# Kernel optimization log

Hardware: AMD Instinct MI355X
Metric: run time of the kernel (lower is better)

The kernel has to match this reference:

```python
import jax, jax.numpy as jnp
import numpy as np

NEG_INF = -1.0e9  # matches torch masked_fill value


def setup_inputs() -> dict:
    key = jax.random.key(0)
    kq, kk, kv, km = jax.random.split(key, 4)
    B, S, D = 16, 2048, 256
    q = jax.random.normal(kq, (B, S, D), dtype=jnp.float32)
    k = jax.random.normal(kk, (B, D, S), dtype=jnp.float32)  # pre-transposed keys
    v = jax.random.normal(kv, (B, S, D), dtype=jnp.float32)
    mask = jax.random.randint(km, (B, 1, S), 0, 2, dtype=jnp.int32)
    return {"q": q, "k": k, "v": v, "mask": mask}


def reference(q, k, v, mask):
    # q: [B, n_q, d], k: [B, d, n_k], v: [B, n_k, n_dv]
    n_dk = k.shape[1]
    att = jnp.matmul(q, k)                      # [B, n_q, n_k]
    att = jnp.where(mask == 0, NEG_INF, att)    # masked_fill(mask==0, -1e9)
    # NOTE: faithful to source — scale applied AFTER softmax
    att = jax.nn.softmax(att, axis=-1) / jnp.asarray(n_dk, att.dtype) ** 0.5
    out = jnp.matmul(att, v)                    # [B, n_q, n_dv]
    return jnp.transpose(out, (0, 2, 1))        # [B, n_dv, n_q]
```

## Files before the change

### kernel.cpp

```cpp
#include <hip/hip_runtime.h>

typedef _Float16 half8 __attribute__((ext_vector_type(8)));
typedef float floatx16 __attribute__((ext_vector_type(16)));

#define B_  16
#define S_  2048
#define D_  256
#define P_RS 40
#define LOG2E 1.4426950408889634f

#define DPP_ROR(x, n) __int_as_float(__builtin_amdgcn_update_dpp( \
    0, __float_as_int(x), 0x120 + (n), 0xf, 0xf, false))

__device__ __forceinline__ float rmax32(float x) {
    x = fmaxf(x, DPP_ROR(x, 1));
    x = fmaxf(x, DPP_ROR(x, 2));
    x = fmaxf(x, DPP_ROR(x, 4));
    x = fmaxf(x, DPP_ROR(x, 8));
    x = fmaxf(x, __shfl_xor(x, 16, 64));
    return x;
}
__device__ __forceinline__ float rsum32(float x) {
    x += DPP_ROR(x, 1);
    x += DPP_ROR(x, 2);
    x += DPP_ROR(x, 4);
    x += DPP_ROR(x, 8);
    x += __shfl_xor(x, 16, 64);
    return x;
}

__device__ __forceinline__ void dma16(const _Float16* g, _Float16* l) {
    __builtin_amdgcn_global_load_lds(
        (const __attribute__((address_space(1))) void*)g,
        (__attribute__((address_space(3))) void*)l, 16, 0, 0);
}

__global__ __launch_bounds__(256)
void tr_swz(const float* __restrict__ in, _Float16* __restrict__ out,
            int Rin, int Cin, int swz)
{
    __shared__ _Float16 tl[64 * 72];
    const int t  = threadIdx.x;
    const int c0 = blockIdx.x * 64, r0 = blockIdx.y * 64;
    const float* ib = in  + (size_t)blockIdx.z * Rin * Cin;
    _Float16*    ob = out + (size_t)blockIdx.z * Rin * Cin;

    const int rr = t >> 4, cc = (t & 15) * 4;
    #pragma unroll
    for (int p = 0; p < 4; ++p) {
        const float4 x = *(const float4*)(ib + (size_t)(r0 + rr + 16*p) * Cin + c0 + cc);
        tl[(cc+0)*72 + rr + 16*p] = (_Float16)x.x;
        tl[(cc+1)*72 + rr + 16*p] = (_Float16)x.y;
        tl[(cc+2)*72 + rr + 16*p] = (_Float16)x.z;
        tl[(cc+3)*72 + rr + 16*p] = (_Float16)x.w;
    }
    __syncthreads();
    #pragma unroll
    for (int u = 0; u < 2; ++u) {
        const int idx  = t + 256*u;
        const int jloc = idx >> 3, lc = idx & 7;
        const half8 h = *(const half8*)(tl + jloc*72 + 8*lc);
        const int jg  = c0 + jloc;
        const int lco = swz ? (lc ^ ((jg >> 1) & 7)) : lc;
        *(half8*)(ob + (size_t)jg * Rin + r0 + 8*lco) = h;
    }
}

__global__ __launch_bounds__(512, 2)
void attn_v7(const float* __restrict__ q, const _Float16* __restrict__ kts,
             const _Float16* __restrict__ vt, const int* __restrict__ mask,
             float* __restrict__ out)
{
    __shared__ _Float16 kb[2][32 * D_];
    __shared__ _Float16 vb[3][32 * D_];
    __shared__ _Float16 pbuf[4][2][32 * P_RS];
    __shared__ float    alb [4][2][32];
    __shared__ float    oscb[4][32];
    __shared__ int      flg [4][2];

    const int tid   = threadIdx.x;
    const int w     = tid >> 6;
    const int isC   = w >> 2;
    const int strip = w & 3;
    const int lane  = tid & 63;
    const int jl    = lane & 31;
    const int h     = lane >> 5;
    const int pj    = (jl >> 1) & 7;

    const int bx   = blockIdx.x;
    const int rest = bx >> 3;
    const int b    = 2 * (bx & 7) + (rest >> 4);
    const int qg   = rest & 15;
    const int i0   = qg * 128 + 32 * strip;

    const float*    qb  = q    + (size_t)b * S_ * D_;
    const _Float16* ktb = kts  + (size_t)b * S_ * D_;
    const _Float16* vtb = vt   + (size_t)b * S_ * D_;
    const int*      mb  = mask + (size_t)b * S_;
    float*          ob  = out  + (size_t)b * D_ * S_;

    if (!isC) {
        const int qv  = (lane & 7) ^ ((lane >> 3) & 7);
        const int vdr = 2 * (lane >> 3) + (qv >> 2);
        const int vco = 8 * (qv & 3);
        const _Float16* vsrc = vtb + (size_t)(64*strip + vdr) * S_ + vco;

        half8 qf[16];
        {
            const float* qrow = qb + (size_t)(i0 + jl) * D_;
            #pragma unroll
            for (int s = 0; s < 16; ++s) {
                const float4 a = *(const float4*)(qrow + 16*s + 8*h);
                const float4 c = *(const float4*)(qrow + 16*s + 8*h + 4);
                half8 v;
                v[0]=(_Float16)a.x; v[1]=(_Float16)a.y; v[2]=(_Float16)a.z; v[3]=(_Float16)a.w;
                v[4]=(_Float16)c.x; v[5]=(_Float16)c.y; v[6]=(_Float16)c.z; v[7]=(_Float16)c.w;
                qf[s] = v;
            }
        }
        float M[16], lsum[16];
        #pragma unroll
        for (int r = 0; r < 16; ++r) { M[r] = -3.0e38f; lsum[r] = 0.0f; }

        #pragma unroll
        for (int m = 0; m < 4; ++m)
            dma16(ktb + (size_t)(8*strip + 2*m) * D_ + lane*8,
                  kb[0] + (8*strip + 2*m) * D_);
        #pragma unroll
        for (int m = 0; m < 4; ++m)
            dma16(vsrc + (size_t)(16*m) * S_, vb[0] + 2048*strip + 512*m);
        __syncthreads();

        int wb = 1;
        for (int t = 0; t < 64; ++t) {
            const int j0 = 32 * t;
            const int jn = ((t + 1) & 63) * 32;
            const _Float16* kcur = kb[t & 1];
            _Float16*       knxt = kb[(t + 1) & 1];

            #pragma unroll
            for (int m = 0; m < 4; ++m)
                dma16(ktb + (size_t)(jn + 8*strip + 2*m) * D_ + lane*8,
                      knxt + (8*strip + 2*m) * D_);
            #pragma unroll
            for (int m = 0; m < 4; ++m)
                dma16(vsrc + jn + (size_t)(16*m) * S_, vb[wb] + 2048*strip + 512*m);
            wb = (wb == 2) ? 0 : wb + 1;

            const float mo = mb[j0 + jl] ? 0.0f : -1.0e9f;

            floatx16 sa = (floatx16){}, sb = (floatx16){};
            #pragma unroll
            for (int s = 0; s < 16; s += 2) {
                const half8 k0 = *(const half8*)(kcur + jl*D_ + 8*((2*s     + h) ^ pj));
                const half8 k1 = *(const half8*)(kcur + jl*D_ + 8*((2*s + 2 + h) ^ pj));
                sa = __builtin_amdgcn_mfma_f32_32x32x16_f16(qf[s],   k0, sa, 0,0,0);
                sb = __builtin_amdgcn_mfma_f32_32x32x16_f16(qf[s+1], k1, sb, 0,0,0);
            }
            float sv[16];
            #pragma unroll
            for (int r = 0; r < 16; ++r) sv[r] = sa[r] + sb[r] + mo;

            float mx = sv[0] - M[0];
            #pragma unroll
            for (int r = 1; r < 16; ++r) mx = fmaxf(mx, sv[r] - M[r]);
            const bool resc = __any(mx > 8.0f);
            if (resc) {
                #pragma unroll
                for (int r = 0; r < 16; ++r) {
                    const float tm = rmax32(sv[r]);
                    const float Mn = fmaxf(M[r], tm);
                    const float al = __builtin_amdgcn_exp2f((M[r] - Mn) * LOG2E);
                    M[r] = Mn;
                    lsum[r] *= al;
                    if (jl == 0) alb[strip][t & 1][(r&3) + 8*(r>>2) + 4*h] = al;
                }
            }
            if (lane == 0) flg[strip][t & 1] = resc ? 1 : 0;

            _Float16* pw = pbuf[strip][t & 1];
            #pragma unroll
            for (int r = 0; r < 16; ++r) {
                const float p = __builtin_amdgcn_exp2f((sv[r] - M[r]) * LOG2E);
                lsum[r] += p;
                pw[((r&3) + 8*(r>>2) + 4*h) * P_RS + jl] = (_Float16)p;
            }
            __syncthreads();
        }

        #pragma unroll
        for (int r = 0; r < 16; ++r) {
            const float osc = 1.0f / (16.0f * rsum32(lsum[r]));
            if (jl == 0) oscb[strip][(r&3) + 8*(r>>2) + 4*h] = osc;
        }
        __syncthreads();
    } else {
        const int gb  = jl >> 1;
        const int swz = gb & 7;
        const int x0  = 4*(jl & 1) + h;
        const int vo0 = gb*64 + ((x0    ) ^ swz)*8;
        const int vo1 = gb*64 + ((x0 ^ 2) ^ swz)*8;

        floatx16 o[8];
        #pragma unroll
        for (int nt = 0; nt < 8; ++nt) o[nt] = (floatx16){};

        auto pv_step = [&](int tt, int vbi) {
            const int buf = tt & 1;
            if (flg[strip][buf]) {
                const float al = alb[strip][buf][jl];
                #pragma unroll
                for (int nt = 0; nt < 8; ++nt)
                    #pragma unroll
                    for (int r = 0; r < 16; ++r) o[nt][r] *= al;
            }
            const _Float16* pw  = pbuf[strip][buf];
            const _Float16* vbt = vb[vbi];
            const half8 pa0 = *(const half8*)(pw + jl*P_RS + 8*h);
            const half8 pa1 = *(const half8*)(pw + jl*P_RS + 16 + 8*h);
            #pragma unroll
            for (int nt = 0; nt < 8; ++nt) {
                const half8 vf0 = *(const half8*)(vbt + 1024*nt + vo0);
                const half8 vf1 = *(const half8*)(vbt + 1024*nt + vo1);
                o[nt] = __builtin_amdgcn_mfma_f32_32x32x16_f16(vf0, pa0, o[nt], 0,0,0);
                o[nt] = __builtin_amdgcn_mfma_f32_32x32x16_f16(vf1, pa1, o[nt], 0,0,0);
            }
        };

        __syncthreads();
        int pvb = 0;
        for (int t = 0; t < 64; ++t) {
            if (t > 0) { pv_step(t - 1, pvb); pvb = (pvb == 2) ? 0 : pvb + 1; }
            __syncthreads();
        }
        pv_step(63, pvb);
        __syncthreads();

        const float oscl = oscb[strip][jl];
        #pragma unroll
        for (int nt = 0; nt < 8; ++nt) {
            #pragma unroll
            for (int r = 0; r < 16; ++r) {
                const int row = (r&3) + 8*(r>>2) + 4*h;
                ob[(size_t)(32*nt + row) * S_ + i0 + jl] = o[nt][r] * oscl;
            }
        }
    }
}

extern "C" void kernel_launch(void* const* d_in, const int* in_sizes, int n_in,
                              void* d_out, int out_size, void* d_ws, size_t ws_size,
                              hipStream_t stream)
{
    const float* q    = (const float*)d_in[0];
    const float* k    = (const float*)d_in[1];
    const float* v    = (const float*)d_in[2];
    const int*   mask = (const int*)d_in[3];
    float*       out  = (float*)d_out;

    _Float16* kt = (_Float16*)d_ws;
    _Float16* vtp = kt + (size_t)B_ * S_ * D_;

    tr_swz<<<dim3(S_/64, D_/64, B_), dim3(256), 0, stream>>>(k, kt, D_, S_, 1);
    tr_swz<<<dim3(D_/64, S_/64, B_), dim3(256), 0, stream>>>(v, vtp, S_, D_, 0);

    attn_v7<<<dim3(B_ * (S_/128)), dim3(512), 0, stream>>>(q, kt, vtp, mask, out);
}
```

Baseline: 305.0 us.

## Deepen K/V prefetch pipeline, split V loads to PV waves, fuse transposes

The attention kernel now prefetches K and V two tiles ahead, using triple-buffered K and quad-buffered V. V loading moves from the score waves to the PV waves, so each wave group fetches only the operand it consumes. Plain __syncthreads is replaced by a barrier that waits only for the older DMA batch (vmcnt(4)), leaving the newest loads in flight across the barrier. The mask is converted once into LDS at kernel start, MFMA sections get raised wave priority, and the two transpose kernels are merged into one launch. In exchange, LDS use rises to roughly 140KB, and the hand-written waitcnt/barrier sequences depend on exact counts of outstanding loads.

```diff
diff --git a/kernel.cpp b/kernel.cpp
--- a/kernel.cpp
+++ b/kernel.cpp
@@ -2,6 +2,7 @@
 
 typedef _Float16 half8 __attribute__((ext_vector_type(8)));
 typedef float floatx16 __attribute__((ext_vector_type(16)));
+typedef int int4v __attribute__((ext_vector_type(4)));
 
 #define B_  16
 #define S_  2048
@@ -35,16 +36,11 @@
         (__attribute__((address_space(3))) void*)l, 16, 0, 0);
 }
 
-__global__ __launch_bounds__(256)
-void tr_swz(const float* __restrict__ in, _Float16* __restrict__ out,
-            int Rin, int Cin, int swz)
+__device__ __forceinline__ void tr_body(const float* __restrict__ ib,
+                                        _Float16* __restrict__ ob,
+                                        int Rin, int Cin, int swz,
+                                        int c0, int r0, _Float16* tl, int t)
 {
-    __shared__ _Float16 tl[64 * 72];
-    const int t  = threadIdx.x;
-    const int c0 = blockIdx.x * 64, r0 = blockIdx.y * 64;
-    const float* ib = in  + (size_t)blockIdx.z * Rin * Cin;
-    _Float16*    ob = out + (size_t)blockIdx.z * Rin * Cin;
-
     const int rr = t >> 4, cc = (t & 15) * 4;
     #pragma unroll
     for (int p = 0; p < 4; ++p) {
@@ -66,14 +62,36 @@
     }
 }
 
+__global__ __launch_bounds__(256)
+void tr_both(const float* __restrict__ k, const float* __restrict__ v,
+             _Float16* __restrict__ kt, _Float16* __restrict__ vtp)
+{
+    __shared__ _Float16 tl[64 * 72];
+    const int id   = blockIdx.x;
+    const int isV  = id >> 11;
+    const int rem  = id & 2047;
+    const int z    = rem >> 7;
+    const int t128 = rem & 127;
+    if (!isV) {
+        const int c0 = (t128 & 31) * 64, r0 = (t128 >> 5) * 64;
+        tr_body(k + (size_t)z * D_ * S_, kt + (size_t)z * S_ * D_,
+                D_, S_, 1, c0, r0, tl, threadIdx.x);
+    } else {
+        const int c0 = (t128 & 3) * 64, r0 = (t128 >> 2) * 64;
+        tr_body(v + (size_t)z * S_ * D_, vtp + (size_t)z * S_ * D_,
+                S_, D_, 0, c0, r0, tl, threadIdx.x);
+    }
+}
+
 __global__ __launch_bounds__(512, 2)
-void attn_v7(const float* __restrict__ q, const _Float16* __restrict__ kts,
+void attn_v8(const float* __restrict__ q, const _Float16* __restrict__ kts,
              const _Float16* __restrict__ vt, const int* __restrict__ mask,
              float* __restrict__ out)
 {
-    __shared__ _Float16 kb[2][32 * D_];
-    __shared__ _Float16 vb[3][32 * D_];
+    __shared__ _Float16 kb[3][32 * D_];
+    __shared__ _Float16 vb[4][32 * D_];
     __shared__ _Float16 pbuf[4][2][32 * P_RS];
+    __shared__ float    mlds[S_];
     __shared__ float    alb [4][2][32];
     __shared__ float    oscb[4][32];
     __shared__ int      flg [4][2];
@@ -99,12 +117,15 @@
     const int*      mb  = mask + (size_t)b * S_;
     float*          ob  = out  + (size_t)b * D_ * S_;
 
+    {
+        const int4v mi = *(const int4v*)(mb + 4*tid);
+        mlds[4*tid+0] = mi[0] ? 0.0f : -1.0e9f;
+        mlds[4*tid+1] = mi[1] ? 0.0f : -1.0e9f;
+        mlds[4*tid+2] = mi[2] ? 0.0f : -1.0e9f;
+        mlds[4*tid+3] = mi[3] ? 0.0f : -1.0e9f;
+    }
+
     if (!isC) {
-        const int qv  = (lane & 7) ^ ((lane >> 3) & 7);
-        const int vdr = 2 * (lane >> 3) + (qv >> 2);
-        const int vco = 8 * (qv & 3);
-        const _Float16* vsrc = vtb + (size_t)(64*strip + vdr) * S_ + vco;
-
         half8 qf[16];
         {
             const float* qrow = qb + (size_t)(i0 + jl) * D_;
@@ -128,28 +149,25 @@
                   kb[0] + (8*strip + 2*m) * D_);
         #pragma unroll
         for (int m = 0; m < 4; ++m)
-            dma16(vsrc + (size_t)(16*m) * S_, vb[0] + 2048*strip + 512*m);
-        __syncthreads();
-
-        int wb = 1;
+            dma16(ktb + (size_t)(32 + 8*strip + 2*m) * D_ + lane*8,
+                  kb[1] + (8*strip + 2*m) * D_);
+        asm volatile("s_waitcnt vmcnt(4) lgkmcnt(0)\n\ts_barrier" ::: "memory");
+
+        int kc = 0, kp = 2;
         for (int t = 0; t < 64; ++t) {
-            const int j0 = 32 * t;
-            const int jn = ((t + 1) & 63) * 32;
-            const _Float16* kcur = kb[t & 1];
-            _Float16*       knxt = kb[(t + 1) & 1];
-
+            const int jexp = ((t + 2) & 63) * 32;
+
+            _Float16* kd = kb[kp];
             #pragma unroll
             for (int m = 0; m < 4; ++m)
-                dma16(ktb + (size_t)(jn + 8*strip + 2*m) * D_ + lane*8,
-                      knxt + (8*strip + 2*m) * D_);
-            #pragma unroll
-            for (int m = 0; m < 4; ++m)
-                dma16(vsrc + jn + (size_t)(16*m) * S_, vb[wb] + 2048*strip + 512*m);
-            wb = (wb == 2) ? 0 : wb + 1;
-
-            const float mo = mb[j0 + jl] ? 0.0f : -1.0e9f;
+                dma16(ktb + (size_t)(jexp + 8*strip + 2*m) * D_ + lane*8,
+                      kd + (8*strip + 2*m) * D_);
+
+            const float mo = mlds[32*t + jl];
+            const _Float16* kcur = kb[kc];
 
             floatx16 sa = (floatx16){}, sb = (floatx16){};
+            __builtin_amdgcn_s_setprio(1);
             #pragma unroll
             for (int s = 0; s < 16; s += 2) {
                 const half8 k0 = *(const half8*)(kcur + jl*D_ + 8*((2*s     + h) ^ pj));
@@ -157,6 +175,7 @@
                 sa = __builtin_amdgcn_mfma_f32_32x32x16_f16(qf[s],   k0, sa, 0,0,0);
                 sb = __builtin_amdgcn_mfma_f32_32x32x16_f16(qf[s+1], k1, sb, 0,0,0);
             }
+            __builtin_amdgcn_s_setprio(0);
             float sv[16];
             #pragma unroll
             for (int r = 0; r < 16; ++r) sv[r] = sa[r] + sb[r] + mo;
@@ -185,7 +204,10 @@
                 lsum[r] += p;
                 pw[((r&3) + 8*(r>>2) + 4*h) * P_RS + jl] = (_Float16)p;
             }
-            __syncthreads();
+
+            asm volatile("s_waitcnt vmcnt(4) lgkmcnt(0)\n\ts_barrier" ::: "memory");
+            kc = (kc == 2) ? 0 : kc + 1;
+            kp = (kp == 2) ? 0 : kp + 1;
         }
 
         #pragma unroll
@@ -193,8 +215,14 @@
             const float osc = 1.0f / (16.0f * rsum32(lsum[r]));
             if (jl == 0) oscb[strip][(r&3) + 8*(r>>2) + 4*h] = osc;
         }
-        __syncthreads();
+        asm volatile("s_waitcnt lgkmcnt(0)\n\ts_barrier" ::: "memory");
+        asm volatile("s_waitcnt vmcnt(0)" ::: "memory");
     } else {
+        const int qv  = (lane & 7) ^ ((lane >> 3) & 7);
+        const int vdr = 2 * (lane >> 3) + (qv >> 2);
+        const int vco = 8 * (qv & 3);
+        const _Float16* vsrc = vtb + (size_t)(64*strip + vdr) * S_ + vco;
+
         const int gb  = jl >> 1;
         const int swz = gb & 7;
         const int x0  = 4*(jl & 1) + h;
@@ -205,7 +233,7 @@
         #pragma unroll
         for (int nt = 0; nt < 8; ++nt) o[nt] = (floatx16){};
 
-        auto pv_step = [&](int tt, int vbi) {
+        auto pv_step = [&](int tt, const _Float16* vbt) {
             const int buf = tt & 1;
             if (flg[strip][buf]) {
                 const float al = alb[strip][buf][jl];
@@ -215,9 +243,9 @@
                     for (int r = 0; r < 16; ++r) o[nt][r] *= al;
             }
             const _Float16* pw  = pbuf[strip][buf];
-            const _Float16* vbt = vb[vbi];
             const half8 pa0 = *(const half8*)(pw + jl*P_RS + 8*h);
             const half8 pa1 = *(const half8*)(pw + jl*P_RS + 16 + 8*h);
+            __builtin_amdgcn_s_setprio(1);
             #pragma unroll
             for (int nt = 0; nt < 8; ++nt) {
                 const half8 vf0 = *(const half8*)(vbt + 1024*nt + vo0);
@@ -225,16 +253,31 @@
                 o[nt] = __builtin_amdgcn_mfma_f32_32x32x16_f16(vf0, pa0, o[nt], 0,0,0);
                 o[nt] = __builtin_amdgcn_mfma_f32_32x32x16_f16(vf1, pa1, o[nt], 0,0,0);
             }
+            __builtin_amdgcn_s_setprio(0);
         };
 
-        __syncthreads();
-        int pvb = 0;
+        #pragma unroll
+        for (int m = 0; m < 4; ++m)
+            dma16(vsrc + (size_t)(16*m) * S_,      vb[0] + 2048*strip + 512*m);
+        #pragma unroll
+        for (int m = 0; m < 4; ++m)
+            dma16(vsrc + 32 + (size_t)(16*m) * S_, vb[1] + 2048*strip + 512*m);
+        asm volatile("s_waitcnt vmcnt(4) lgkmcnt(0)\n\ts_barrier" ::: "memory");
+
         for (int t = 0; t < 64; ++t) {
-            if (t > 0) { pv_step(t - 1, pvb); pvb = (pvb == 2) ? 0 : pvb + 1; }
-            __syncthreads();
-        }
-        pv_step(63, pvb);
-        __syncthreads();
+            const int jexp = ((t + 2) & 63) * 32;
+
+            _Float16* vd = vb[(t + 2) & 3];
+            #pragma unroll
+            for (int m = 0; m < 4; ++m)
+                dma16(vsrc + jexp + (size_t)(16*m) * S_, vd + 2048*strip + 512*m);
+
+            if (t > 0) pv_step(t - 1, vb[(t - 1) & 3]);
+
+            asm volatile("s_waitcnt vmcnt(4) lgkmcnt(0)\n\ts_barrier" ::: "memory");
+        }
+        pv_step(63, vb[63 & 3]);
+        asm volatile("s_waitcnt lgkmcnt(0)\n\ts_barrier" ::: "memory");
 
         const float oscl = oscb[strip][jl];
         #pragma unroll
@@ -245,6 +288,7 @@
                 ob[(size_t)(32*nt + row) * S_ + i0 + jl] = o[nt][r] * oscl;
             }
         }
+        asm volatile("s_waitcnt vmcnt(0)" ::: "memory");
     }
 }
 
@@ -261,8 +305,6 @@
     _Float16* kt = (_Float16*)d_ws;
     _Float16* vtp = kt + (size_t)B_ * S_ * D_;
 
-    tr_swz<<<dim3(S_/64, D_/64, B_), dim3(256), 0, stream>>>(k, kt, D_, S_, 1);
-    tr_swz<<<dim3(D_/64, S_/64, B_), dim3(256), 0, stream>>>(v, vtp, S_, D_, 0);
-
-    attn_v7<<<dim3(B_ * (S_/128)), dim3(512), 0, stream>>>(q, kt, vtp, mask, out);
-}
+    tr_both<<<dim3(4096), dim3(256), 0, stream>>>(k, v, kt, vtp);
+    attn_v8<<<dim3(B_ * (S_/128)), dim3(512), 0, stream>>>(q, kt, vtp, mask, out);
+}
```

Result: faster. 293.4 us (-3.8%).
